# Kernel tuning notes

Hardware: AMD Instinct MI355X
Metric: run time of the kernel (lower is better)

## Reference

```python
import jax, jax.numpy as jnp
import numpy as np

NBITS = 4  # asymmetric fake-quant

def fake_quant_asym(w, bit):
    # mask of nonzero weights (zeros stay zero after quantization)
    mask = (w != 0).astype(w.dtype)
    max_ = jnp.max(w)
    min_ = jnp.min(w)
    alpha = max_ - min_
    beta = min_
    step = (2 ** bit) - 1
    ws = (w - beta) / alpha
    R = jnp.round(step * ws) / step
    wq = alpha * R + beta
    return wq * mask

def setup_inputs() -> dict:
    key = jax.random.key(0)
    k1, k2, k3 = jax.random.split(key, 3)
    m, n = 1024, 1024
    std = np.sqrt(2.0 / (m + n))
    x = jax.random.normal(k1, (16384, m), dtype=jnp.float32)
    weight = jax.random.normal(k2, (n, m), dtype=jnp.float32) * std
    bias = jax.random.normal(k3, (n,), dtype=jnp.float32) * 0.01
    return {"x": x, "weight": weight, "bias": bias}

def reference(x, weight, bias):
    wq = fake_quant_asym(weight, NBITS)
    # F.linear: y = x @ W^T + b
    return jnp.einsum('tm,nm->tn', x, wq) + bias
```

## Files before the change

kernel.cpp:

```cpp
#include <hip/hip_runtime.h>

#define M_DIM 16384
#define N_DIM 1024
#define K_DIM 1024

typedef short v8s __attribute__((ext_vector_type(8)));
typedef float v4f __attribute__((ext_vector_type(4)));
typedef unsigned v2u __attribute__((ext_vector_type(2)));

__device__ __forceinline__ unsigned short f2bf(float f) {
  unsigned u = __float_as_uint(f);
  unsigned r = (u + 0x7FFFu + ((u >> 16) & 1u)) >> 16;
  return (unsigned short)r;
}

__device__ __forceinline__ void gload16(const void* g, void* l) {
  __builtin_amdgcn_global_load_lds(
      (const __attribute__((address_space(1))) void*)g,
      (__attribute__((address_space(3))) void*)l, 16, 0, 0);
}

#define DSR(dst, addr, off) \
  asm volatile("ds_read_b128 %0, %1 offset:" off : "=v"(dst) : "v"(addr))

__global__ void wminmax_part(const float* __restrict__ w, float* __restrict__ part) {
  int tid = blockIdx.x * 256 + threadIdx.x;
  float mx = -3.402823466e38f, mn = 3.402823466e38f;
  for (int i = tid; i < N_DIM * K_DIM / 4; i += 256 * 256) {
    float4 v = *(const float4*)(w + i * 4);
    mx = fmaxf(fmaxf(mx, fmaxf(v.x, v.y)), fmaxf(v.z, v.w));
    mn = fminf(fminf(mn, fminf(v.x, v.y)), fminf(v.z, v.w));
  }
  #pragma unroll
  for (int o = 32; o > 0; o >>= 1) {
    mx = fmaxf(mx, __shfl_down(mx, o));
    mn = fminf(mn, __shfl_down(mn, o));
  }
  __shared__ float smx[4], smn[4];
  int lane = threadIdx.x & 63, wv = threadIdx.x >> 6;
  if (lane == 0) { smx[wv] = mx; smn[wv] = mn; }
  __syncthreads();
  if (threadIdx.x == 0) {
    mx = fmaxf(fmaxf(smx[0], smx[1]), fmaxf(smx[2], smx[3]));
    mn = fminf(fminf(smn[0], smn[1]), fminf(smn[2], smn[3]));
    part[blockIdx.x] = mx;
    part[256 + blockIdx.x] = mn;
  }
}

__global__ void wminmax_final(const float* __restrict__ part, float* __restrict__ mm) {
  float mx = part[threadIdx.x];
  float mn = part[256 + threadIdx.x];
  #pragma unroll
  for (int o = 32; o > 0; o >>= 1) {
    mx = fmaxf(mx, __shfl_down(mx, o));
    mn = fminf(mn, __shfl_down(mn, o));
  }
  __shared__ float smx[4], smn[4];
  int lane = threadIdx.x & 63, wv = threadIdx.x >> 6;
  if (lane == 0) { smx[wv] = mx; smn[wv] = mn; }
  __syncthreads();
  if (threadIdx.x == 0) {
    mm[0] = fmaxf(fmaxf(smx[0], smx[1]), fmaxf(smx[2], smx[3]));
    mm[1] = fminf(fminf(smn[0], smn[1]), fminf(smn[2], smn[3]));
  }
}

__global__ void quant_kernel(const float* __restrict__ w, const float* __restrict__ mm,
                             unsigned short* __restrict__ wq) {
  const float mx = mm[0], mn = mm[1];
  const float alpha = mx - mn, beta = mn;
  int i = (blockIdx.x * 256 + threadIdx.x) * 4;
  float4 v = *(const float4*)(w + i);
  float f[4] = {v.x, v.y, v.z, v.w};
  ushort4 o;
  unsigned short ov[4];
  #pragma unroll
  for (int j = 0; j < 4; j++) {
    float s = (f[j] - beta) / alpha;
    float R = rintf(15.0f * s) / 15.0f;
    float q = alpha * R + beta;
    if (f[j] == 0.0f) q = 0.0f;
    ov[j] = f2bf(q);
  }
  o.x = ov[0]; o.y = ov[1]; o.z = ov[2]; o.w = ov[3];
  *(ushort4*)(wq + i) = o;
}

__global__ __launch_bounds__(512, 2) void gemm_fused(
    const float* __restrict__ x, const unsigned short* __restrict__ wq,
    const float* __restrict__ bias, float* __restrict__ out) {
  __shared__ __attribute__((aligned(16))) unsigned short As[2][256][32];
  __shared__ __attribute__((aligned(16))) unsigned short Bs[4][256][32];

  const int tid = threadIdx.x;
  const int lane = tid & 63;
  const int wv = tid >> 6;
  const int wr = wv >> 2;
  const int wc = wv & 3;
  const int bm = blockIdx.x;
  const int bn = blockIdx.y;

  const int srow = wv * 32 + (lane >> 2);
  const int ssw = ((lane & 3) ^ ((lane >> 3) & 3)) * 8;
  const unsigned short* bS = wq + (size_t)(bn * 256 + srow) * K_DIM + ssw;

  const float* aF = x + (size_t)(bm * 256 + wv * 32 + (lane >> 3)) * K_DIM + (lane & 7) * 4;

  const int frow = lane & 15;
  const int fsw = ((lane >> 4) ^ ((frow >> 1) & 3)) * 8;
  const unsigned ldsA0 =
      (unsigned)(unsigned long long)(__attribute__((address_space(3))) unsigned short*)&As[0][0][0];
  const unsigned ldsB0 =
      (unsigned)(unsigned long long)(__attribute__((address_space(3))) unsigned short*)&Bs[0][0][0];
  const unsigned aLane = ldsA0 + (unsigned)((wr * 128 + frow) * 32 + fsw) * 2u;
  const unsigned bLane = ldsB0 + (unsigned)((wc * 64 + frow) * 32 + fsw) * 2u;

  const unsigned wA = ldsA0 +
      (unsigned)((wv * 32 + (lane >> 3)) * 64 +
                 ((((lane & 7) >> 1) ^ ((lane >> 4) & 3)) * 16) + ((lane & 7) & 1) * 8);

  v4f acc[8][4];
  #pragma unroll
  for (int m = 0; m < 8; m++)
    #pragma unroll
    for (int n = 0; n < 4; n++) acc[m][n] = (v4f)(0.0f);

  v8s af[4], bf[4];
  float4 ra0[4], ra1[4];

#define RA_LOAD(RA_, H2_) do { \
    _Pragma("unroll") \
    for (int j_ = 0; j_ < 4; j_++) \
      RA_[j_] = *(const float4*)(aF + (size_t)(H2_) * 32 + j_ * 8 * K_DIM); \
  } while (0)

#define CVTW(RA_, SL_) do { \
    _Pragma("unroll") \
    for (int j_ = 0; j_ < 4; j_++) { \
      v2u p_; \
      p_.x = (unsigned)f2bf(RA_[j_].x) | ((unsigned)f2bf(RA_[j_].y) << 16); \
      p_.y = (unsigned)f2bf(RA_[j_].z) | ((unsigned)f2bf(RA_[j_].w) << 16); \
      asm volatile("ds_write_b64 %0, %1" \
                   :: "v"(wA + (SL_) * 16384u + j_ * 512u), "v"(p_) : "memory"); \
    } \
  } while (0)

#define STAGE_B(H_, SL_) do { \
    gload16(bS + (size_t)(H_) * 32, &Bs[SL_][wv * 32][0]); \
    gload16(bS + (size_t)(H_) * 32 + 16 * K_DIM, &Bs[SL_][wv * 32 + 16][0]); \
  } while (0)

#define MM16(MH_) do { \
    _Pragma("unroll") \
    for (int i_ = 0; i_ < 4; i_++) \
      _Pragma("unroll") \
      for (int n_ = 0; n_ < 4; n_++) \
        acc[(MH_) * 4 + i_][n_] = __builtin_amdgcn_mfma_f32_16x16x32_bf16( \
            af[i_], bf[n_], acc[(MH_) * 4 + i_][n_], 0, 0, 0); \
  } while (0)

#define PH0(H_, AS_, BS_, RALD_, STG_) do { \
    const unsigned aP = aLane + (AS_) * 16384u; \
    const unsigned bP = bLane + (BS_) * 16384u; \
    DSR(af[0], aP, "0");    DSR(af[1], aP, "1024"); \
    DSR(af[2], aP, "2048"); DSR(af[3], aP, "3072"); \
    DSR(bf[0], bP, "0");    DSR(bf[1], bP, "1024"); \
    DSR(bf[2], bP, "2048"); DSR(bf[3], bP, "3072"); \
    if (STG_) RA_LOAD(RALD_, (H_) + 2); \
    __builtin_amdgcn_s_barrier(); \
    asm volatile("s_waitcnt lgkmcnt(0)" ::: "memory"); \
    __builtin_amdgcn_sched_barrier(0); \
    __builtin_amdgcn_s_setprio(1); \
    MM16(0); \
    __builtin_amdgcn_s_setprio(0); \
    __builtin_amdgcn_s_barrier(); \
  } while (0)

#define PH1(H_, AS_, BW_, RACV_, STG_, CVT_, GATE_) do { \
    const unsigned aP = aLane + (AS_) * 16384u + 4096u; \
    DSR(af[0], aP, "0");    DSR(af[1], aP, "1024"); \
    DSR(af[2], aP, "2048"); DSR(af[3], aP, "3072"); \
    if (CVT_) CVTW(RACV_, (AS_) ^ 1); \
    if (STG_) STAGE_B((H_) + 2, BW_); \
    __builtin_amdgcn_s_barrier(); \
    asm volatile("s_waitcnt lgkmcnt(0)" ::: "memory"); \
    __builtin_amdgcn_sched_barrier(0); \
    __builtin_amdgcn_s_setprio(1); \
    MM16(1); \
    __builtin_amdgcn_s_setprio(0); \
    asm volatile("s_waitcnt vmcnt(" GATE_ ")" ::: "memory"); \
    __builtin_amdgcn_s_barrier(); \
  } while (0)

#define KHALF(H_, AS_, BS_, BW_, RALD_, RACV_, STG_, CVT_, GATE_) do { \
    PH0(H_, AS_, BS_, RALD_, STG_); \
    PH1(H_, AS_, BW_, RACV_, STG_, CVT_, GATE_); \
  } while (0)

  RA_LOAD(ra0, 0);
  RA_LOAD(ra1, 1);
  STAGE_B(0, 0);
  STAGE_B(1, 1);
  CVTW(ra0, 0);
  asm volatile("s_waitcnt vmcnt(2)" ::: "memory");
  asm volatile("s_waitcnt lgkmcnt(0)" ::: "memory");
  __builtin_amdgcn_s_barrier();

  #pragma unroll 1
  for (int kh = 0; kh < 28; kh += 4) {
    KHALF(kh + 0, 0, 0, 2, ra0, ra1, 1, 1, "6");
    KHALF(kh + 1, 1, 1, 3, ra1, ra0, 1, 1, "6");
    KHALF(kh + 2, 0, 2, 0, ra0, ra1, 1, 1, "6");
    KHALF(kh + 3, 1, 3, 1, ra1, ra0, 1, 1, "6");
  }
  KHALF(28, 0, 0, 2, ra0, ra1, 1, 1, "6");
  KHALF(29, 1, 1, 3, ra1, ra0, 1, 1, "6");
  KHALF(30, 0, 2, 0, ra0, ra1, 0, 1, "0");
  KHALF(31, 1, 3, 0, ra1, ra0, 0, 0, "0");

#undef KHALF
#undef PH0
#undef PH1
#undef MM16
#undef STAGE_B
#undef CVTW
#undef RA_LOAD

  const int colbase = bn * 256 + wc * 64;
  const int rowbase = bm * 256 + wr * 128;
  #pragma unroll
  for (int n = 0; n < 4; n++) {
    const int col = colbase + n * 16 + (lane & 15);
    const float bv = bias[col];
    #pragma unroll
    for (int m = 0; m < 8; m++) {
      const int row0 = rowbase + m * 16 + (lane >> 4) * 4;
      #pragma unroll
      for (int r = 0; r < 4; r++)
        out[(size_t)(row0 + r) * N_DIM + col] = acc[m][n][r] + bv;
    }
  }
}

__global__ __launch_bounds__(256) void gemm_kernel(
    const float* __restrict__ x, const unsigned short* __restrict__ wq,
    const float* __restrict__ bias, float* __restrict__ out) {
  __shared__ __attribute__((aligned(16))) unsigned short As[2][128][32];
  __shared__ __attribute__((aligned(16))) unsigned short Bs[2][128][32];

  const int tid = threadIdx.x;
  const int lane = tid & 63;
  const int wv = tid >> 6;
  const int wr = wv >> 1, wc = wv & 1;
  const int bm = blockIdx.x, bn = blockIdx.y;

  const int arow = tid >> 1;
  const int acol = (tid & 1) << 4;
  const float* aptr = x + (size_t)(bm * 128 + arow) * K_DIM + acol;
  const int fA = (arow >> 1) & 3;
  const int ac0 = (tid & 1) * 2;
  const int aw0 = ((ac0) ^ fA) * 8;
  const int aw1 = ((ac0 + 1) ^ fA) * 8;

  const int brow0 = wv * 32 + (lane >> 2);
  const int bsrcc = (lane & 3) ^ ((lane >> 3) & 3);
  const unsigned short* bptr0 = wq + (size_t)(bn * 128 + brow0) * K_DIM + bsrcc * 8;
  const unsigned short* bptr1 = bptr0 + (size_t)16 * K_DIM;

  v4f acc[4][4];
  #pragma unroll
  for (int i = 0; i < 4; i++)
    #pragma unroll
    for (int j = 0; j < 4; j++) acc[i][j] = (v4f)(0.0f);

  const int frow = lane & 15;
  const int fkc = lane >> 4;
  const int fsw = (fkc ^ ((frow >> 1) & 3)) * 8;

  float4 areg[4];
  #pragma unroll
  for (int j = 0; j < 4; j++) areg[j] = *(const float4*)(aptr + j * 4);

  {
    const float* f = (const float*)areg;
    union { v8s v; unsigned short u[8]; } cv0, cv1;
    #pragma unroll
    for (int i = 0; i < 8; i++) { cv0.u[i] = f2bf(f[i]); cv1.u[i] = f2bf(f[i + 8]); }
    *(v8s*)&As[0][arow][aw0] = cv0.v;
    *(v8s*)&As[0][arow][aw1] = cv1.v;
    gload16(bptr0, &Bs[0][wv * 32][0]);
    gload16(bptr1, &Bs[0][wv * 32 + 16][0]);
  }
  #pragma unroll
  for (int j = 0; j < 4; j++) areg[j] = *(const float4*)(aptr + 32 + j * 4);
  __syncthreads();

  for (int kt = 0; kt < K_DIM / 32; ++kt) {
    const int cur = kt & 1, nxt = cur ^ 1;
    if (kt + 1 < K_DIM / 32) {
      const float* f = (const float*)areg;
      union { v8s v; unsigned short u[8]; } cv0, cv1;
      #pragma unroll
      for (int i = 0; i < 8; i++) { cv0.u[i] = f2bf(f[i]); cv1.u[i] = f2bf(f[i + 8]); }
      *(v8s*)&As[nxt][arow][aw0] = cv0.v;
      *(v8s*)&As[nxt][arow][aw1] = cv1.v;
      gload16(bptr0 + (size_t)(kt + 1) * 32, &Bs[nxt][wv * 32][0]);
      gload16(bptr1 + (size_t)(kt + 1) * 32, &Bs[nxt][wv * 32 + 16][0]);
      if (kt + 2 < K_DIM / 32) {
        const float* ap = aptr + (kt + 2) * 32;
        #pragma unroll
        for (int j = 0; j < 4; j++) areg[j] = *(const float4*)(ap + j * 4);
      }
    }
    v8s af[4], bf[4];
    #pragma unroll
    for (int m = 0; m < 4; m++)
      af[m] = *(const v8s*)&As[cur][wr * 64 + m * 16 + frow][fsw];
    #pragma unroll
    for (int n = 0; n < 4; n++)
      bf[n] = *(const v8s*)&Bs[cur][wc * 64 + n * 16 + frow][fsw];
    #pragma unroll
    for (int m = 0; m < 4; m++)
      #pragma unroll
      for (int n = 0; n < 4; n++)
        acc[m][n] = __builtin_amdgcn_mfma_f32_16x16x32_bf16(af[m], bf[n], acc[m][n], 0, 0, 0);
    __syncthreads();
  }

  const int colbase = bn * 128 + wc * 64;
  const int rowbase = bm * 128 + wr * 64;
  #pragma unroll
  for (int n = 0; n < 4; n++) {
    const int col = colbase + n * 16 + (lane & 15);
    const float bv = bias[col];
    #pragma unroll
    for (int m = 0; m < 4; m++) {
      const int row0 = rowbase + m * 16 + (lane >> 4) * 4;
      #pragma unroll
      for (int r = 0; r < 4; r++)
        out[(size_t)(row0 + r) * N_DIM + col] = acc[m][n][r] + bv;
    }
  }
}

extern "C" void kernel_launch(void* const* d_in, const int* in_sizes, int n_in,
                              void* d_out, int out_size, void* d_ws, size_t ws_size,
                              hipStream_t stream) {
  const float* x = (const float*)d_in[0];
  const float* wt = (const float*)d_in[1];
  const float* bias = (const float*)d_in[2];
  float* out = (float*)d_out;

  float* part = (float*)d_ws;
  float* mm = part + 512;
  unsigned short* wqbuf = (unsigned short*)((char*)d_ws + 4096);
  const size_t need = 4096 + 2ull * 1024 * 1024;

  wminmax_part<<<256, 256, 0, stream>>>(wt, part);
  wminmax_final<<<1, 256, 0, stream>>>(part, mm);
  quant_kernel<<<1024, 256, 0, stream>>>(wt, mm, wqbuf);

  if (ws_size >= need) {
    dim3 grid(M_DIM / 256, N_DIM / 256);
    gemm_fused<<<grid, 512, 0, stream>>>(x, wqbuf, bias, out);
  } else {
    dim3 grid(M_DIM / 128, N_DIM / 128);
    gemm_kernel<<<grid, 256, 0, stream>>>(x, wqbuf, bias, out);
  }
}
```

Before: 66.69 us.

## Fuse weight min/max reduction and quantization into one grid-synchronized kernel

```diff
diff --git a/kernel.cpp b/kernel.cpp
--- a/kernel.cpp
+++ b/kernel.cpp
@@ -23,13 +23,26 @@
 #define DSR(dst, addr, off) \
   asm volatile("ds_read_b128 %0, %1 offset:" off : "=v"(dst) : "v"(addr))
 
-__global__ void wminmax_part(const float* __restrict__ w, float* __restrict__ part) {
-  int tid = blockIdx.x * 256 + threadIdx.x;
+__device__ __forceinline__ unsigned fkey(float f) {
+  unsigned u = __float_as_uint(f);
+  return (u & 0x80000000u) ? ~u : (u | 0x80000000u);
+}
+__device__ __forceinline__ float fdec(unsigned k) {
+  unsigned u = (k & 0x80000000u) ? (k ^ 0x80000000u) : ~k;
+  return __uint_as_float(u);
+}
+
+__global__ void prep_kernel(const float* __restrict__ w,
+                            unsigned short* __restrict__ wq,
+                            unsigned* __restrict__ sync) {
+  const int b = blockIdx.x, t = threadIdx.x;
+  float4 v[4];
   float mx = -3.402823466e38f, mn = 3.402823466e38f;
-  for (int i = tid; i < N_DIM * K_DIM / 4; i += 256 * 256) {
-    float4 v = *(const float4*)(w + i * 4);
-    mx = fmaxf(fmaxf(mx, fmaxf(v.x, v.y)), fmaxf(v.z, v.w));
-    mn = fminf(fminf(mn, fminf(v.x, v.y)), fminf(v.z, v.w));
+  #pragma unroll
+  for (int k = 0; k < 4; k++) {
+    v[k] = *(const float4*)(w + (size_t)(b * 1024 + k * 256 + t) * 4);
+    mx = fmaxf(fmaxf(mx, fmaxf(v[k].x, v[k].y)), fmaxf(v[k].z, v[k].w));
+    mn = fminf(fminf(mn, fminf(v[k].x, v[k].y)), fminf(v[k].z, v[k].w));
   }
   #pragma unroll
   for (int o = 32; o > 0; o >>= 1) {
@@ -37,54 +50,41 @@
     mn = fminf(mn, __shfl_down(mn, o));
   }
   __shared__ float smx[4], smn[4];
-  int lane = threadIdx.x & 63, wv = threadIdx.x >> 6;
+  __shared__ float sab[2];
+  const int lane = t & 63, wv = t >> 6;
   if (lane == 0) { smx[wv] = mx; smn[wv] = mn; }
   __syncthreads();
-  if (threadIdx.x == 0) {
+  if (t == 0) {
     mx = fmaxf(fmaxf(smx[0], smx[1]), fmaxf(smx[2], smx[3]));
     mn = fminf(fminf(smn[0], smn[1]), fminf(smn[2], smn[3]));
-    part[blockIdx.x] = mx;
-    part[256 + blockIdx.x] = mn;
-  }
-}
-
-__global__ void wminmax_final(const float* __restrict__ part, float* __restrict__ mm) {
-  float mx = part[threadIdx.x];
-  float mn = part[256 + threadIdx.x];
-  #pragma unroll
-  for (int o = 32; o > 0; o >>= 1) {
-    mx = fmaxf(mx, __shfl_down(mx, o));
-    mn = fminf(mn, __shfl_down(mn, o));
-  }
-  __shared__ float smx[4], smn[4];
-  int lane = threadIdx.x & 63, wv = threadIdx.x >> 6;
-  if (lane == 0) { smx[wv] = mx; smn[wv] = mn; }
+    atomicMax(&sync[0], fkey(mx));
+    atomicMax(&sync[1], fkey(-mn));
+    __threadfence();
+    atomicAdd(&sync[2], 1u);
+    while (atomicAdd(&sync[2], 0u) < 256u) {}
+    const float fmx = fdec(atomicAdd(&sync[0], 0u));
+    const float fmn = -fdec(atomicAdd(&sync[1], 0u));
+    sab[0] = fmx - fmn;
+    sab[1] = fmn;
+  }
   __syncthreads();
-  if (threadIdx.x == 0) {
-    mm[0] = fmaxf(fmaxf(smx[0], smx[1]), fmaxf(smx[2], smx[3]));
-    mm[1] = fminf(fminf(smn[0], smn[1]), fminf(smn[2], smn[3]));
-  }
-}
-
-__global__ void quant_kernel(const float* __restrict__ w, const float* __restrict__ mm,
-                             unsigned short* __restrict__ wq) {
-  const float mx = mm[0], mn = mm[1];
-  const float alpha = mx - mn, beta = mn;
-  int i = (blockIdx.x * 256 + threadIdx.x) * 4;
-  float4 v = *(const float4*)(w + i);
-  float f[4] = {v.x, v.y, v.z, v.w};
-  ushort4 o;
-  unsigned short ov[4];
-  #pragma unroll
-  for (int j = 0; j < 4; j++) {
-    float s = (f[j] - beta) / alpha;
-    float R = rintf(15.0f * s) / 15.0f;
-    float q = alpha * R + beta;
-    if (f[j] == 0.0f) q = 0.0f;
-    ov[j] = f2bf(q);
-  }
-  o.x = ov[0]; o.y = ov[1]; o.z = ov[2]; o.w = ov[3];
-  *(ushort4*)(wq + i) = o;
+  const float alpha = sab[0], beta = sab[1];
+  #pragma unroll
+  for (int k = 0; k < 4; k++) {
+    float f[4] = {v[k].x, v[k].y, v[k].z, v[k].w};
+    ushort4 o;
+    unsigned short ov[4];
+    #pragma unroll
+    for (int j = 0; j < 4; j++) {
+      float s = (f[j] - beta) / alpha;
+      float R = rintf(15.0f * s) / 15.0f;
+      float q = alpha * R + beta;
+      if (f[j] == 0.0f) q = 0.0f;
+      ov[j] = f2bf(q);
+    }
+    o.x = ov[0]; o.y = ov[1]; o.z = ov[2]; o.w = ov[3];
+    *(ushort4*)(wq + (size_t)(b * 1024 + k * 256 + t) * 4) = o;
+  }
 }
 
 __global__ __launch_bounds__(512, 2) void gemm_fused(
@@ -352,14 +352,12 @@
   const float* bias = (const float*)d_in[2];
   float* out = (float*)d_out;
 
-  float* part = (float*)d_ws;
-  float* mm = part + 512;
+  unsigned* sync = (unsigned*)d_ws;
   unsigned short* wqbuf = (unsigned short*)((char*)d_ws + 4096);
   const size_t need = 4096 + 2ull * 1024 * 1024;
 
-  wminmax_part<<<256, 256, 0, stream>>>(wt, part);
-  wminmax_final<<<1, 256, 0, stream>>>(part, mm);
-  quant_kernel<<<1024, 256, 0, stream>>>(wt, mm, wqbuf);
+  hipMemsetAsync(d_ws, 0, 16, stream);
+  prep_kernel<<<256, 256, 0, stream>>>(wt, wqbuf, sync);
 
   if (ws_size >= need) {
     dim3 grid(M_DIM / 256, N_DIM / 256);
```

Result: slower. 76.93 us (+15.4%).
